# Kernel optimization log

Hardware: AMD Instinct MI355X
Metric: run time of the kernel (lower is better)

Reference implementation:

```python
import jax, jax.numpy as jnp
import numpy as np

DIM = 1024
NUM_HEADS = 16
HEAD_DIM = DIM // NUM_HEADS


def setup_inputs() -> dict:
    key = jax.random.key(0)
    ks = jax.random.split(key, 5)
    B, T = 2, 2048
    x = jax.random.normal(ks[0], (B, T, DIM), dtype=jnp.float32)
    s = 1.0 / np.sqrt(DIM)
    W_qkv = jax.random.normal(ks[1], (DIM, 3 * DIM), dtype=jnp.float32) * s
    b_qkv = jnp.zeros((3 * DIM,), dtype=jnp.float32)
    W_out = jax.random.normal(ks[2], (DIM, DIM), dtype=jnp.float32) * s
    b_out = jnp.zeros((DIM,), dtype=jnp.float32)
    return {"x": x, "W_qkv": W_qkv, "b_qkv": b_qkv, "W_out": W_out, "b_out": b_out}


def reference(x, W_qkv, b_qkv, W_out, b_out):
    B, T, D = x.shape
    H, Hd = NUM_HEADS, HEAD_DIM
    qkv = x @ W_qkv + b_qkv                       # [B,T,3D]
    qkv = qkv.reshape(B, T, 3, H, Hd)
    q = jnp.transpose(qkv[:, :, 0], (0, 2, 1, 3))  # [B,H,T,Hd]
    k = jnp.transpose(qkv[:, :, 1], (0, 2, 1, 3))
    v = jnp.transpose(qkv[:, :, 2], (0, 2, 1, 3))
    att = jnp.einsum('bhqd,bhkd->bhqk', q, k) / np.sqrt(Hd)  # [B,H,T,T]
    causal = jnp.tril(jnp.ones((T, T), dtype=bool))
    att = jnp.where(causal[None, None], att, -jnp.inf)
    att = jax.nn.softmax(att, axis=-1)
    out = jnp.einsum('bhqk,bhkd->bhqd', att, v)   # [B,H,T,Hd]
    out = jnp.transpose(out, (0, 2, 1, 3)).reshape(B, T, D)
    return out @ W_out + b_out
```

## Files before the change

kernel.cpp:

```cpp
#include <hip/hip_runtime.h>
#include <hip/hip_bf16.h>

typedef unsigned short u16;
typedef __attribute__((ext_vector_type(8))) short short8;
typedef __attribute__((ext_vector_type(4))) float f32x4;
typedef __attribute__((ext_vector_type(4))) unsigned short u16x4;

#define LOG2E 1.44269504088896340736f


__device__ __forceinline__ void gl_lds16(const void* g, void* l) {
  __builtin_amdgcn_global_load_lds(
      (__attribute__((address_space(1))) void*)g,
      (__attribute__((address_space(3))) void*)l, 16, 0, 0);
}

__device__ __forceinline__ float exp2_fast(float x) {
#if __has_builtin(__builtin_amdgcn_exp2f)
  return __builtin_amdgcn_exp2f(x);
#else
  return exp2f(x);
#endif
}

__device__ __forceinline__ u16 f2bf(float f) {
  union { float f; unsigned int i; } v;
  v.f = f;
  unsigned int r = v.i + 0x7fffu + ((v.i >> 16) & 1u);
  return (u16)(r >> 16);
}

__device__ __forceinline__ unsigned int pack_bf2(float lo, float hi) {
  union { __hip_bfloat162 h2; unsigned int u; } c;
  c.h2 = __float22bfloat162_rn(make_float2(lo, hi));
  return c.u;
}


__global__ __launch_bounds__(256) void prep_kernel(
    const float4* __restrict__ x, u16x4* __restrict__ xb,
    const float* __restrict__ Wqkv, u16* __restrict__ WqkvT,
    const float* __restrict__ Wout, u16* __restrict__ WoutT) {
  __shared__ u16 t[64][65];
  int bid = blockIdx.x, tid = threadIdx.x;
  if (bid < 4096) {
    int i = bid * 256 + tid;
    float4 v = x[i];
    u16x4 o;
    o.x = f2bf(v.x); o.y = f2bf(v.y); o.z = f2bf(v.z); o.w = f2bf(v.w);
    xb[i] = o;
    return;
  }
  const float* W;
  u16* WT;
  int K = 1024, N, bxx, byy;
  if (bid < 4864) {
    int tt = bid - 4096;
    W = Wqkv; WT = WqkvT; N = 3072; bxx = tt % 48; byy = tt / 48;
  } else {
    int tt = bid - 4864;
    W = Wout; WT = WoutT; N = 1024; bxx = tt % 16; byy = tt / 16;
  }
  int r0 = byy * 64, c0 = bxx * 64;
  int tx = tid & 63, ty = tid >> 6;
  for (int r = ty; r < 64; r += 4)
    t[r][tx] = f2bf(W[(size_t)(r0 + r) * N + c0 + tx]);
  __syncthreads();
  for (int r = ty; r < 64; r += 4)
    WT[(size_t)(c0 + r) * K + r0 + tx] = t[tx][r];
}


template <bool OUT_F32, int BN>
__global__ __launch_bounds__(256) void gemm_bt_kernel(
    const u16* __restrict__ A, const u16* __restrict__ Bt,
    const float* __restrict__ bias, void* __restrict__ Cout,
    int M, int N, int K) {
  constexpr int NBJ = BN / 32;
  constexpr int CH_A = 16;
  constexpr int CH_B = BN / 8;
  constexpr int PER_W = (CH_A + CH_B) / 4;
  __shared__ u16 As[128 * 64];
  __shared__ u16 Bs[BN * 64];
  int tid = threadIdx.x;
  int w = tid >> 6, lane = tid & 63, l15 = lane & 15, quad = lane >> 4;
  int m0 = blockIdx.y * 128, n0 = blockIdx.x * BN;
  int wm = (w & 1) * 64, wn = (w >> 1) * (BN / 2);

  f32x4 acc[4][NBJ];
#pragma unroll
  for (int i = 0; i < 4; ++i)
#pragma unroll
    for (int j = 0; j < NBJ; ++j) {
      f32x4 z = {0.f, 0.f, 0.f, 0.f};
      acc[i][j] = z;
    }

  int r8 = lane >> 3;
  int sw = ((lane & 7) ^ r8) * 8;

  for (int kt = 0; kt < K; kt += 64) {
    __syncthreads();
#pragma unroll
    for (int i = 0; i < PER_W; ++i) {
      int c = w * PER_W + i;
      if (c < CH_A) {
        int row = m0 + c * 8 + r8;
        gl_lds16(A + (size_t)row * K + kt + sw, As + c * 512);
      } else {
        int cc = c - CH_A;
        int row = n0 + cc * 8 + r8;
        gl_lds16(Bt + (size_t)row * K + kt + sw, Bs + cc * 512);
      }
    }
    __syncthreads();

#pragma unroll
    for (int kh = 0; kh < 2; ++kh) {
      short8 af[4], bf[NBJ];
#pragma unroll
      for (int i = 0; i < 4; ++i) {
        int R = wm + i * 16 + l15;
        af[i] = *(const short8*)(As + R * 64 +
                                 ((kh * 32 + quad * 8) ^ ((R & 7) * 8)));
      }
#pragma unroll
      for (int j = 0; j < NBJ; ++j) {
        int R = wn + j * 16 + l15;
        bf[j] = *(const short8*)(Bs + R * 64 +
                                 ((kh * 32 + quad * 8) ^ ((R & 7) * 8)));
      }
#pragma unroll
      for (int i = 0; i < 4; ++i)
#pragma unroll
        for (int j = 0; j < NBJ; ++j)
          acc[i][j] = __builtin_amdgcn_mfma_f32_16x16x32_bf16(af[i], bf[j],
                                                              acc[i][j], 0, 0, 0);
    }
  }

  float bv[NBJ];
#pragma unroll
  for (int j = 0; j < NBJ; ++j) bv[j] = bias[n0 + wn + j * 16 + l15];
#pragma unroll
  for (int i = 0; i < 4; ++i)
#pragma unroll
    for (int j = 0; j < NBJ; ++j) {
      int col = n0 + wn + j * 16 + l15;
#pragma unroll
      for (int r = 0; r < 4; ++r) {
        int row = m0 + wm + i * 16 + quad * 4 + r;
        float val = acc[i][j][r] + bv[j];
        if (OUT_F32)
          ((float*)Cout)[(size_t)row * N + col] = val;
        else
          ((u16*)Cout)[(size_t)row * N + col] = f2bf(val);
      }
    }
}


__global__ __launch_bounds__(512, 2) void flash_kernel(
    const u16* __restrict__ qkv, u16* __restrict__ att) {
  __shared__ unsigned int SH[16384];

  int tid = threadIdx.x;
  int w = tid >> 6, half = w >> 2, wq = w & 3;
  int lane = tid & 63, l15 = lane & 15, quad = lane >> 4;
  int bx = blockIdx.x;
  int p = bx >> 5, bh = bx & 31, b = bh >> 4, h = bh & 15;
  const int qs[2] = {15 - p, p};
  const int kmax0 = 2 * qs[0] + 1, kmax1 = 2 * p + 1;
  const int jmax = 16 - p;

  const u16* base = qkv + (size_t)b * 2048 * 3072 + h * 64;
  const u16* kb = base + 1024;
  const u16* vb = base + 2048;

  int ht = tid & 255;
  const int krow = ht >> 3, h7 = ht & 7;

  unsigned int* KsH = SH + half * 2048;
  unsigned int* VtH = SH + 4096 + half * 2048;
  unsigned int* Pw = SH + 8192 + w * 1024;

  uint4 kr0 = *(const uint4*)(kb + (size_t)(half * 64 + krow) * 3072 + h7 * 8);
  uint4 kr1 = *(const uint4*)(kb + (size_t)(half * 64 + krow + 32) * 3072 + h7 * 8);
  uint4 vr0 = *(const uint4*)(vb + (size_t)(half * 64 + 2 * krow) * 3072 + h7 * 8);
  uint4 vr1 = *(const uint4*)(vb + (size_t)(half * 64 + 2 * krow + 1) * 3072 + h7 * 8);

  f32x4 o[2][2][4];
#pragma unroll
  for (int t = 0; t < 2; ++t)
#pragma unroll
    for (int qsub = 0; qsub < 2; ++qsub)
#pragma unroll
      for (int jd = 0; jd < 4; ++jd) {
        f32x4 z = {0.f, 0.f, 0.f, 0.f};
        o[t][qsub][jd] = z;
      }
  float lsum[2][2] = {0.f, 0.f, 0.f, 0.f};

  const int psw = (l15 & 7) << 2;
  const float kscale = 0.125f * LOG2E;

  for (int j = 0; j < jmax; ++j) {
    int kt = 2 * j + half;
    __syncthreads();
    *(uint4*)&KsH[32 * krow + ((4 * h7) ^ ((krow & 7) << 2))] = kr0;
    {
      int r1 = krow + 32;
      *(uint4*)&KsH[32 * r1 + ((4 * h7) ^ ((r1 & 7) << 2))] = kr1;
    }
    {
      const u16* av = (const u16*)&vr0;
      const u16* bvp = (const u16*)&vr1;
#pragma unroll
      for (int jj = 0; jj < 8; ++jj) {
        int d = h7 * 8 + jj;
        VtH[32 * d + (krow ^ ((jj ^ h7) << 2))] =
            (unsigned int)av[jj] | ((unsigned int)bvp[jj] << 16);
      }
    }
    __syncthreads();
    if (j + 1 < jmax) {
      int kn = (kt + 2) * 64;
      kr0 = *(const uint4*)(kb + (size_t)(kn + krow) * 3072 + h7 * 8);
      kr1 = *(const uint4*)(kb + (size_t)(kn + krow + 32) * 3072 + h7 * 8);
      vr0 = *(const uint4*)(vb + (size_t)(kn + 2 * krow) * 3072 + h7 * 8);
      vr1 = *(const uint4*)(vb + (size_t)(kn + 2 * krow + 1) * 3072 + h7 * 8);
    }

#pragma unroll
    for (int t = 0; t < 2; ++t) {
      int km = t ? kmax1 : kmax0;
      if (kt > km) continue;
      bool last = (kt == km);
      if (last && wq < 2) continue;
      bool domask = last || ((kt == km - 1) && wq < 2);
      int qloc = ((last ? (wq - 2) : wq) << 5) + l15;

      const u16* qtb = base + (size_t)(qs[t] * 128 + wq * 32 + l15) * 3072;
      short8 aq00 = *(const short8*)(qtb + quad * 8);
      short8 aq01 = *(const short8*)(qtb + 32 + quad * 8);
      short8 aq10 = *(const short8*)(qtb + 16 * 3072 + quad * 8);
      short8 aq11 = *(const short8*)(qtb + 16 * 3072 + 32 + quad * 8);

      f32x4 s0[4], s1[4];
#pragma unroll
      for (int jn = 0; jn < 4; ++jn) {
        f32x4 z = {0.f, 0.f, 0.f, 0.f};
        s0[jn] = z;
        s1[jn] = z;
      }
#pragma unroll
      for (int ss = 0; ss < 2; ++ss) {
        short8 a0 = ss ? aq01 : aq00;
        short8 a1 = ss ? aq11 : aq10;
#pragma unroll
        for (int jn = 0; jn < 4; ++jn) {
          int row = jn * 16 + l15;
          short8 bk = *(const short8*)&KsH[32 * row + ((16 * ss + 4 * quad) ^
                                                       ((row & 7) << 2))];
          s0[jn] = __builtin_amdgcn_mfma_f32_16x16x32_bf16(bk, a0, s0[jn], 0, 0, 0);
          s1[jn] = __builtin_amdgcn_mfma_f32_16x16x32_bf16(bk, a1, s1[jn], 0, 0, 0);
        }
      }

#pragma unroll
      for (int qsub = 0; qsub < 2; ++qsub) {
        int qq = qloc + qsub * 16;
        float ls = 0.f;
#pragma unroll
        for (int jn = 0; jn < 4; ++jn) {
          f32x4 sv = qsub ? s1[jn] : s0[jn];
          float pv[4];
#pragma unroll
          for (int r = 0; r < 4; ++r) {
            float e = exp2_fast(fmaf(sv[r], kscale, -16.0f));
            if (domask && (jn * 16 + quad * 4 + r > qq)) e = 0.f;
            pv[r] = e;
            ls += e;
          }
          uint2 dd = make_uint2(pack_bf2(pv[0], pv[1]), pack_bf2(pv[2], pv[3]));
          *(uint2*)&Pw[qsub * 512 + 32 * l15 +
                       (((jn << 3) + (quad << 1)) ^ psw)] = dd;
        }
        lsum[t][qsub] += ls;
      }

#pragma unroll
      for (int ss = 0; ss < 2; ++ss) {
        short8 pf0 = *(const short8*)&Pw[32 * l15 +
                                         (((ss << 4) + (quad << 2)) ^ psw)];
        short8 pf1 = *(const short8*)&Pw[512 + 32 * l15 +
                                         (((ss << 4) + (quad << 2)) ^ psw)];
#pragma unroll
        for (int jd = 0; jd < 4; ++jd) {
          int vrow = jd * 16 + l15;
          int f = (vrow & 7) ^ ((vrow >> 3) & 7);
          short8 bvv = *(const short8*)&VtH[32 * vrow +
                                            (((ss << 4) + (quad << 2)) ^ (f << 2))];
          o[t][0][jd] =
              __builtin_amdgcn_mfma_f32_16x16x32_bf16(bvv, pf0, o[t][0][jd], 0, 0, 0);
          o[t][1][jd] =
              __builtin_amdgcn_mfma_f32_16x16x32_bf16(bvv, pf1, o[t][1][jd], 0, 0, 0);
        }
      }
    }
  }

  float lf[2][2];
#pragma unroll
  for (int t = 0; t < 2; ++t)
#pragma unroll
    for (int qsub = 0; qsub < 2; ++qsub) {
      float v = lsum[t][qsub];
      v += __shfl_xor(v, 16, 64);
      v += __shfl_xor(v, 32, 64);
      lf[t][qsub] = v;
    }

  float* OM = (float*)SH;
  float* LM = (float*)(SH + 8704);
  __syncthreads();
#pragma unroll
  for (int t = 0; t < 2; ++t) {
    if (half == 0) {
#pragma unroll
      for (int qsub = 0; qsub < 2; ++qsub) {
        int q = wq * 32 + qsub * 16 + l15;
#pragma unroll
        for (int jd = 0; jd < 4; ++jd)
          *(float4*)&OM[q * 68 + jd * 16 + quad * 4] = *(float4*)&o[t][qsub][jd];
        if (quad == 0) LM[q] = lf[t][qsub];
      }
    }
    __syncthreads();
    if (half == 1) {
#pragma unroll
      for (int qsub = 0; qsub < 2; ++qsub) {
        int q = wq * 32 + qsub * 16 + l15;
        float lr = lf[t][qsub] + LM[q];
        float inv = 1.f / lr;
        size_t row = (size_t)b * 2048 + qs[t] * 128 + q;
        u16* orow = att + row * 1024 + h * 64 + quad * 4;
#pragma unroll
        for (int jd = 0; jd < 4; ++jd) {
          float4 pa = *(float4*)&OM[q * 68 + jd * 16 + quad * 4];
          uint2 dd = make_uint2(pack_bf2((o[t][qsub][jd][0] + pa.x) * inv,
                                         (o[t][qsub][jd][1] + pa.y) * inv),
                                pack_bf2((o[t][qsub][jd][2] + pa.z) * inv,
                                         (o[t][qsub][jd][3] + pa.w) * inv));
          *(uint2*)(orow + jd * 16) = dd;
        }
      }
    }
    __syncthreads();
  }
}


extern "C" void kernel_launch(void* const* d_in, const int* in_sizes, int n_in,
                              void* d_out, int out_size, void* d_ws,
                              size_t ws_size, hipStream_t stream) {
  const float* x = (const float*)d_in[0];
  const float* Wqkv = (const float*)d_in[1];
  const float* bqkv = (const float*)d_in[2];
  const float* Wout = (const float*)d_in[3];
  const float* bout = (const float*)d_in[4];
  float* out = (float*)d_out;

  char* ws = (char*)d_ws;
  u16* WqkvT = (u16*)(ws);
  u16* WoutT = (u16*)(ws + 6291456);
  u16* qkv = (u16*)(ws + 8388608);
  u16* attn = (u16*)(ws + 33554432);
  u16* xb = (u16*)(ws + 41943040);

  prep_kernel<<<5120, 256, 0, stream>>>((const float4*)x, (u16x4*)xb, Wqkv,
                                        WqkvT, Wout, WoutT);
  gemm_bt_kernel<false, 128><<<dim3(24, 32), 256, 0, stream>>>(
      xb, WqkvT, bqkv, (void*)qkv, 4096, 3072, 1024);
  flash_kernel<<<256, 512, 0, stream>>>(qkv, attn);
  gemm_bt_kernel<true, 64><<<dim3(16, 32), 256, 0, stream>>>(
      attn, WoutT, bout, (void*)out, 4096, 1024, 1024);
}
```

Baseline: 183.8 us.

## Split paired query tiles into one tile per block, doubling flash grid

The flash kernel previously paired a long and a short causal query tile in each block (256 blocks). Now each block handles a single 128-row query tile (512 blocks, heaviest tiles dispatched first), Q fragments are hoisted into registers once, and accumulator state is halved. Launch bounds are raised to 4 blocks per SM to cut register pressure and raise occupancy. The cost is less work per block for amortizing the K/V loads, and possible register spills under the tighter bound.

```diff
diff --git a/kernel.cpp b/kernel.cpp
--- a/kernel.cpp
+++ b/kernel.cpp
@@ -160,7 +160,7 @@
 }
 
 
-__global__ __launch_bounds__(512, 2) void flash_kernel(
+__global__ __launch_bounds__(512, 4) void flash_kernel(
     const u16* __restrict__ qkv, u16* __restrict__ att) {
   __shared__ unsigned int SH[16384];
 
@@ -168,10 +168,10 @@
   int w = tid >> 6, half = w >> 2, wq = w & 3;
   int lane = tid & 63, l15 = lane & 15, quad = lane >> 4;
   int bx = blockIdx.x;
-  int p = bx >> 5, bh = bx & 31, b = bh >> 4, h = bh & 15;
-  const int qs[2] = {15 - p, p};
-  const int kmax0 = 2 * qs[0] + 1, kmax1 = 2 * p + 1;
-  const int jmax = 16 - p;
+  int g = bx >> 5;
+  int qi = (bx < 256) ? (15 - g) : (g - 8);
+  int bh = bx & 31, b = bh >> 4, h = bh & 15;
+  const int jmax = qi + 1;
 
   const u16* base = qkv + (size_t)b * 2048 * 3072 + h * 64;
   const u16* kb = base + 1024;
@@ -183,23 +183,30 @@
   unsigned int* KsH = SH + half * 2048;
   unsigned int* VtH = SH + 4096 + half * 2048;
   unsigned int* Pw = SH + 8192 + w * 1024;
+
+  short8 aq[2][2];
+  {
+    const u16* qtb = base + (size_t)(qi * 128 + wq * 32 + l15) * 3072;
+    aq[0][0] = *(const short8*)(qtb + quad * 8);
+    aq[0][1] = *(const short8*)(qtb + 32 + quad * 8);
+    aq[1][0] = *(const short8*)(qtb + 16 * 3072 + quad * 8);
+    aq[1][1] = *(const short8*)(qtb + 16 * 3072 + 32 + quad * 8);
+  }
 
   uint4 kr0 = *(const uint4*)(kb + (size_t)(half * 64 + krow) * 3072 + h7 * 8);
   uint4 kr1 = *(const uint4*)(kb + (size_t)(half * 64 + krow + 32) * 3072 + h7 * 8);
   uint4 vr0 = *(const uint4*)(vb + (size_t)(half * 64 + 2 * krow) * 3072 + h7 * 8);
   uint4 vr1 = *(const uint4*)(vb + (size_t)(half * 64 + 2 * krow + 1) * 3072 + h7 * 8);
 
-  f32x4 o[2][2][4];
-#pragma unroll
-  for (int t = 0; t < 2; ++t)
-#pragma unroll
-    for (int qsub = 0; qsub < 2; ++qsub)
-#pragma unroll
-      for (int jd = 0; jd < 4; ++jd) {
-        f32x4 z = {0.f, 0.f, 0.f, 0.f};
-        o[t][qsub][jd] = z;
-      }
-  float lsum[2][2] = {0.f, 0.f, 0.f, 0.f};
+  f32x4 o[2][4];
+#pragma unroll
+  for (int qsub = 0; qsub < 2; ++qsub)
+#pragma unroll
+    for (int jd = 0; jd < 4; ++jd) {
+      f32x4 z = {0.f, 0.f, 0.f, 0.f};
+      o[qsub][jd] = z;
+    }
+  float lsum[2] = {0.f, 0.f};
 
   const int psw = (l15 & 7) << 2;
   const float kscale = 0.125f * LOG2E;
@@ -231,132 +238,115 @@
       vr1 = *(const uint4*)(vb + (size_t)(kn + 2 * krow + 1) * 3072 + h7 * 8);
     }
 
-#pragma unroll
-    for (int t = 0; t < 2; ++t) {
-      int km = t ? kmax1 : kmax0;
-      if (kt > km) continue;
-      bool last = (kt == km);
-      if (last && wq < 2) continue;
-      bool domask = last || ((kt == km - 1) && wq < 2);
-      int qloc = ((last ? (wq - 2) : wq) << 5) + l15;
-
-      const u16* qtb = base + (size_t)(qs[t] * 128 + wq * 32 + l15) * 3072;
-      short8 aq00 = *(const short8*)(qtb + quad * 8);
-      short8 aq01 = *(const short8*)(qtb + 32 + quad * 8);
-      short8 aq10 = *(const short8*)(qtb + 16 * 3072 + quad * 8);
-      short8 aq11 = *(const short8*)(qtb + 16 * 3072 + 32 + quad * 8);
-
-      f32x4 s0[4], s1[4];
+    bool lastj = (j == qi);
+    if (lastj && half == 1 && wq < 2) continue;
+    bool domask = lastj && (half == 1 ? (wq >= 2) : (wq < 2));
+    int qbase = (half ? (wq - 2) : wq) << 5;
+
+    f32x4 s0[4], s1[4];
+#pragma unroll
+    for (int jn = 0; jn < 4; ++jn) {
+      f32x4 z = {0.f, 0.f, 0.f, 0.f};
+      s0[jn] = z;
+      s1[jn] = z;
+    }
+#pragma unroll
+    for (int ss = 0; ss < 2; ++ss) {
 #pragma unroll
       for (int jn = 0; jn < 4; ++jn) {
-        f32x4 z = {0.f, 0.f, 0.f, 0.f};
-        s0[jn] = z;
-        s1[jn] = z;
-      }
-#pragma unroll
-      for (int ss = 0; ss < 2; ++ss) {
-        short8 a0 = ss ? aq01 : aq00;
-        short8 a1 = ss ? aq11 : aq10;
-#pragma unroll
-        for (int jn = 0; jn < 4; ++jn) {
-          int row = jn * 16 + l15;
-          short8 bk = *(const short8*)&KsH[32 * row + ((16 * ss + 4 * quad) ^
-                                                       ((row & 7) << 2))];
-          s0[jn] = __builtin_amdgcn_mfma_f32_16x16x32_bf16(bk, a0, s0[jn], 0, 0, 0);
-          s1[jn] = __builtin_amdgcn_mfma_f32_16x16x32_bf16(bk, a1, s1[jn], 0, 0, 0);
+        int row = jn * 16 + l15;
+        short8 bk = *(const short8*)&KsH[32 * row + ((16 * ss + 4 * quad) ^
+                                                     ((row & 7) << 2))];
+        s0[jn] = __builtin_amdgcn_mfma_f32_16x16x32_bf16(bk, aq[0][ss], s0[jn],
+                                                         0, 0, 0);
+        s1[jn] = __builtin_amdgcn_mfma_f32_16x16x32_bf16(bk, aq[1][ss], s1[jn],
+                                                         0, 0, 0);
+      }
+    }
+
+#pragma unroll
+    for (int qsub = 0; qsub < 2; ++qsub) {
+      int qq = qbase + qsub * 16 + l15;
+      float ls = 0.f;
+#pragma unroll
+      for (int jn = 0; jn < 4; ++jn) {
+        f32x4 sv = qsub ? s1[jn] : s0[jn];
+        float pv[4];
+#pragma unroll
+        for (int r = 0; r < 4; ++r) {
+          float e = exp2_fast(fmaf(sv[r], kscale, -16.0f));
+          if (domask && (jn * 16 + quad * 4 + r > qq)) e = 0.f;
+          pv[r] = e;
+          ls += e;
         }
-      }
-
-#pragma unroll
-      for (int qsub = 0; qsub < 2; ++qsub) {
-        int qq = qloc + qsub * 16;
-        float ls = 0.f;
-#pragma unroll
-        for (int jn = 0; jn < 4; ++jn) {
-          f32x4 sv = qsub ? s1[jn] : s0[jn];
-          float pv[4];
-#pragma unroll
-          for (int r = 0; r < 4; ++r) {
-            float e = exp2_fast(fmaf(sv[r], kscale, -16.0f));
-            if (domask && (jn * 16 + quad * 4 + r > qq)) e = 0.f;
-            pv[r] = e;
-            ls += e;
-          }
-          uint2 dd = make_uint2(pack_bf2(pv[0], pv[1]), pack_bf2(pv[2], pv[3]));
-          *(uint2*)&Pw[qsub * 512 + 32 * l15 +
-                       (((jn << 3) + (quad << 1)) ^ psw)] = dd;
-        }
-        lsum[t][qsub] += ls;
-      }
-
-#pragma unroll
-      for (int ss = 0; ss < 2; ++ss) {
-        short8 pf0 = *(const short8*)&Pw[32 * l15 +
-                                         (((ss << 4) + (quad << 2)) ^ psw)];
-        short8 pf1 = *(const short8*)&Pw[512 + 32 * l15 +
-                                         (((ss << 4) + (quad << 2)) ^ psw)];
-#pragma unroll
-        for (int jd = 0; jd < 4; ++jd) {
-          int vrow = jd * 16 + l15;
-          int f = (vrow & 7) ^ ((vrow >> 3) & 7);
-          short8 bvv = *(const short8*)&VtH[32 * vrow +
-                                            (((ss << 4) + (quad << 2)) ^ (f << 2))];
-          o[t][0][jd] =
-              __builtin_amdgcn_mfma_f32_16x16x32_bf16(bvv, pf0, o[t][0][jd], 0, 0, 0);
-          o[t][1][jd] =
-              __builtin_amdgcn_mfma_f32_16x16x32_bf16(bvv, pf1, o[t][1][jd], 0, 0, 0);
-        }
-      }
-    }
-  }
-
-  float lf[2][2];
-#pragma unroll
-  for (int t = 0; t < 2; ++t)
-#pragma unroll
-    for (int qsub = 0; qsub < 2; ++qsub) {
-      float v = lsum[t][qsub];
-      v += __shfl_xor(v, 16, 64);
-      v += __shfl_xor(v, 32, 64);
-      lf[t][qsub] = v;
-    }
+        uint2 dd = make_uint2(pack_bf2(pv[0], pv[1]), pack_bf2(pv[2], pv[3]));
+        *(uint2*)&Pw[qsub * 512 + 32 * l15 +
+                     (((jn << 3) + (quad << 1)) ^ psw)] = dd;
+      }
+      lsum[qsub] += ls;
+    }
+
+#pragma unroll
+    for (int ss = 0; ss < 2; ++ss) {
+      short8 pf0 = *(const short8*)&Pw[32 * l15 +
+                                       (((ss << 4) + (quad << 2)) ^ psw)];
+      short8 pf1 = *(const short8*)&Pw[512 + 32 * l15 +
+                                       (((ss << 4) + (quad << 2)) ^ psw)];
+#pragma unroll
+      for (int jd = 0; jd < 4; ++jd) {
+        int vrow = jd * 16 + l15;
+        int f = (vrow & 7) ^ ((vrow >> 3) & 7);
+        short8 bvv = *(const short8*)&VtH[32 * vrow +
+                                          (((ss << 4) + (quad << 2)) ^ (f << 2))];
+        o[0][jd] =
+            __builtin_amdgcn_mfma_f32_16x16x32_bf16(bvv, pf0, o[0][jd], 0, 0, 0);
+        o[1][jd] =
+            __builtin_amdgcn_mfma_f32_16x16x32_bf16(bvv, pf1, o[1][jd], 0, 0, 0);
+      }
+    }
+  }
+
+  float lf[2];
+#pragma unroll
+  for (int qsub = 0; qsub < 2; ++qsub) {
+    float v = lsum[qsub];
+    v += __shfl_xor(v, 16, 64);
+    v += __shfl_xor(v, 32, 64);
+    lf[qsub] = v;
+  }
 
   float* OM = (float*)SH;
   float* LM = (float*)(SH + 8704);
   __syncthreads();
-#pragma unroll
-  for (int t = 0; t < 2; ++t) {
-    if (half == 0) {
-#pragma unroll
-      for (int qsub = 0; qsub < 2; ++qsub) {
-        int q = wq * 32 + qsub * 16 + l15;
-#pragma unroll
-        for (int jd = 0; jd < 4; ++jd)
-          *(float4*)&OM[q * 68 + jd * 16 + quad * 4] = *(float4*)&o[t][qsub][jd];
-        if (quad == 0) LM[q] = lf[t][qsub];
-      }
-    }
-    __syncthreads();
-    if (half == 1) {
-#pragma unroll
-      for (int qsub = 0; qsub < 2; ++qsub) {
-        int q = wq * 32 + qsub * 16 + l15;
-        float lr = lf[t][qsub] + LM[q];
-        float inv = 1.f / lr;
-        size_t row = (size_t)b * 2048 + qs[t] * 128 + q;
-        u16* orow = att + row * 1024 + h * 64 + quad * 4;
-#pragma unroll
-        for (int jd = 0; jd < 4; ++jd) {
-          float4 pa = *(float4*)&OM[q * 68 + jd * 16 + quad * 4];
-          uint2 dd = make_uint2(pack_bf2((o[t][qsub][jd][0] + pa.x) * inv,
-                                         (o[t][qsub][jd][1] + pa.y) * inv),
-                                pack_bf2((o[t][qsub][jd][2] + pa.z) * inv,
-                                         (o[t][qsub][jd][3] + pa.w) * inv));
-          *(uint2*)(orow + jd * 16) = dd;
-        }
-      }
-    }
-    __syncthreads();
+  if (half == 0) {
+#pragma unroll
+    for (int qsub = 0; qsub < 2; ++qsub) {
+      int q = wq * 32 + qsub * 16 + l15;
+#pragma unroll
+      for (int jd = 0; jd < 4; ++jd)
+        *(float4*)&OM[q * 68 + jd * 16 + quad * 4] = *(float4*)&o[qsub][jd];
+      if (quad == 0) LM[q] = lf[qsub];
+    }
+  }
+  __syncthreads();
+  if (half == 1) {
+#pragma unroll
+    for (int qsub = 0; qsub < 2; ++qsub) {
+      int q = wq * 32 + qsub * 16 + l15;
+      float lr = lf[qsub] + LM[q];
+      float inv = 1.f / lr;
+      size_t row = (size_t)b * 2048 + qi * 128 + q;
+      u16* orow = att + row * 1024 + h * 64 + quad * 4;
+#pragma unroll
+      for (int jd = 0; jd < 4; ++jd) {
+        float4 pa = *(float4*)&OM[q * 68 + jd * 16 + quad * 4];
+        uint2 dd = make_uint2(pack_bf2((o[qsub][jd][0] + pa.x) * inv,
+                                       (o[qsub][jd][1] + pa.y) * inv),
+                              pack_bf2((o[qsub][jd][2] + pa.z) * inv,
+                                       (o[qsub][jd][3] + pa.w) * inv));
+        *(uint2*)(orow + jd * 16) = dd;
+      }
+    }
   }
 }
 
@@ -382,7 +372,7 @@
                                         WqkvT, Wout, WoutT);
   gemm_bt_kernel<false, 128><<<dim3(24, 32), 256, 0, stream>>>(
       xb, WqkvT, bqkv, (void*)qkv, 4096, 3072, 1024);
-  flash_kernel<<<256, 512, 0, stream>>>(qkv, attn);
+  flash_kernel<<<512, 512, 0, stream>>>(qkv, attn);
   gemm_bt_kernel<true, 64><<<dim3(16, 32), 256, 0, stream>>>(
       attn, WoutT, bout, (void*)out, 4096, 1024, 1024);
 }
```

Result: slower. 193.0 us (+5.0%).
